# Kernel tuning notes

Hardware: AMD Instinct MI355X
Metric: run time of the kernel (lower is better)

## Reference

```python
import jax, jax.numpy as jnp
import numpy as np

B, C, H, W = 32, 256, 56, 56
NH, WS, SS = 8, 7, 3
N = WS * WS
EPS = 1e-5


def _rel_pos_index(ws):
    ch, cw = np.meshgrid(np.arange(ws), np.arange(ws), indexing='ij')
    coords = np.stack([ch.reshape(-1), cw.reshape(-1)])  # (2, N)
    rel = coords[:, :, None] - coords[:, None, :]        # (2, N, N)
    rel = rel.transpose(1, 2, 0)
    rel[:, :, 0] += ws - 1
    rel[:, :, 1] += ws - 1
    rel[:, :, 0] *= 2 * ws - 1
    return rel.sum(-1)  # (N, N) int


def _attn_mask(Hh, Ww, ws, ss):
    img = np.zeros((Hh, Ww), dtype=np.float32)
    cnt = 0
    for hs in (slice(0, -ws), slice(-ws, -ss), slice(-ss, None)):
        for wsl in (slice(0, -ws), slice(-ws, -ss), slice(-ss, None)):
            img[hs, wsl] = cnt
            cnt += 1
    mw = img.reshape(Hh // ws, ws, Ww // ws, ws).transpose(0, 2, 1, 3).reshape(-1, ws * ws)
    am = mw[:, None, :] - mw[:, :, None]
    return np.where(am != 0, np.float32(-100.0), np.float32(0.0))  # (nW, N, N)

RPI = _rel_pos_index(WS)
AMASK = _attn_mask(H, W, WS, SS)


def _ln(x, w, b):
    mu = x.mean(-1, keepdims=True)
    var = ((x - mu) ** 2).mean(-1, keepdims=True)
    return (x - mu) * jax.lax.rsqrt(var + EPS) * w + b


def setup_inputs() -> dict:
    key = jax.random.key(0)
    ks = jax.random.split(key, 10)
    s = 0.02
    return {
        'x': jax.random.normal(ks[0], (B, C, H, W), jnp.float32),
        'qkv_w': jax.random.normal(ks[1], (3 * C, C), jnp.float32) * s,
        'q_bias': jnp.zeros((C,), jnp.float32),
        'v_bias': jnp.zeros((C,), jnp.float32),
        'proj_w': jax.random.normal(ks[2], (C, C), jnp.float32) * s,
        'proj_b': jnp.zeros((C,), jnp.float32),
        'rpb_table': jax.random.normal(ks[3], ((2 * WS - 1) * (2 * WS - 1), NH), jnp.float32) * s,
        'norm1_w': jnp.ones((C,), jnp.float32),
        'norm1_b': jnp.zeros((C,), jnp.float32),
        'norm2_w': jnp.ones((C,), jnp.float32),
        'norm2_b': jnp.zeros((C,), jnp.float32),
        'fc1_w': jax.random.normal(ks[4], (4 * C, C), jnp.float32) * s,
        'fc1_b': jnp.zeros((4 * C,), jnp.float32),
        'fc2_w': jax.random.normal(ks[5], (C, 4 * C), jnp.float32) * s,
        'fc2_b': jnp.zeros((C,), jnp.float32),
    }


def reference(x, qkv_w, q_bias, v_bias, proj_w, proj_b, rpb_table,
              norm1_w, norm1_b, norm2_w, norm2_b, fc1_w, fc1_b, fc2_w, fc2_b):
    b = x.shape[0]
    hd = C // NH
    scale = hd ** -0.5
    nWh, nWw = H // WS, W // WS
    nW = nWh * nWw

    # (B,C,H,W) -> (B, L, C)
    xs = x.transpose(0, 2, 3, 1).reshape(b, H * W, C)
    shortcut = xs
    xn = _ln(xs, norm1_w, norm1_b).reshape(b, H, W, C)
    # cyclic shift
    xn = jnp.roll(xn, (-SS, -SS), axis=(1, 2))
    # window partition -> (B*nW, N, C)
    xw = xn.reshape(b, nWh, WS, nWw, WS, C).transpose(0, 1, 3, 2, 4, 5).reshape(b * nW, N, C)

    qkv_bias = jnp.concatenate([q_bias, jnp.zeros_like(v_bias), v_bias])
    qkv = xw @ qkv_w.T + qkv_bias                      # (B_, N, 3C)
    qkv = qkv.reshape(b * nW, N, 3, NH, hd).transpose(2, 0, 3, 1, 4)
    q, k, v = qkv[0], qkv[1], qkv[2]                   # (B_, NH, N, hd)

    attn = jnp.einsum('whnd,whmd->whnm', q * scale, k)  # (B_, NH, N, N)
    bias = rpb_table[RPI.reshape(-1)].reshape(N, N, NH).transpose(2, 0, 1)
    attn = attn + bias[None]
    attn = attn.reshape(b, nW, NH, N, N) + jnp.asarray(AMASK)[None, :, None]
    attn = jax.nn.softmax(attn.reshape(b * nW, NH, N, N), axis=-1)

    out = jnp.einsum('whnm,whmd->whnd', attn, v)        # (B_, NH, N, hd)
    out = out.transpose(0, 2, 1, 3).reshape(b * nW, N, C)
    out = out @ proj_w.T + proj_b

    # window reverse + un-shift
    out = out.reshape(b, nWh, nWw, WS, WS, C).transpose(0, 1, 3, 2, 4, 5).reshape(b, H, W, C)
    out = jnp.roll(out, (SS, SS), axis=(1, 2)).reshape(b, H * W, C)

    xs = shortcut + out
    h = _ln(xs, norm2_w, norm2_b)
    h = jax.nn.relu(h @ fc1_w.T + fc1_b) @ fc2_w.T + fc2_b
    xs = xs + h
    return xs.reshape(b, H, W, C).transpose(0, 3, 1, 2)
```

## Files before the change

kernel.cpp:

```cpp
#include <hip/hip_runtime.h>
#include <math.h>

#define EPS 1e-5f

constexpr int Bc = 32, Cc = 256, Hc = 56, Wc = 56;
constexpr int NHc = 8, HDc = 32, WSc = 7, SSc = 3;
constexpr int NTOK = 49;
constexpr int NWIN = 64;
constexpr int Lc = Hc * Wc;
constexpr int Mrows = Bc * NWIN * NTOK;
constexpr int GIMG = 16;
constexpr int NGRP = Bc / GIMG;
constexpr int ROWS_G = GIMG * Lc;
constexpr int WIN_G = GIMG * NWIN;

typedef short bf16x8 __attribute__((ext_vector_type(8)));
typedef float f32x4 __attribute__((ext_vector_type(4)));
typedef unsigned short u16x8 __attribute__((ext_vector_type(8)));
typedef unsigned short u16x4 __attribute__((ext_vector_type(4)));

__device__ __forceinline__ float bf2f(unsigned short u) {
    return __uint_as_float(((unsigned)u) << 16);
}
__device__ __forceinline__ unsigned short f2bf(float f) {
    unsigned x = __float_as_uint(f);
    return (unsigned short)((x + 0x7fffu + ((x >> 16) & 1u)) >> 16);
}
__device__ __forceinline__ void gload_lds16(const void* g, void* l) {
    __builtin_amdgcn_global_load_lds(
        (const __attribute__((address_space(1))) unsigned int*)g,
        (__attribute__((address_space(3))) unsigned int*)l, 16, 0, 0);
}
__device__ __forceinline__ void inv_swz(int bp, int& row, int& ch) {
    int b2 = ((bp >> 2) ^ (bp >> 4)) & 1;
    int b1_ = ((bp >> 1) ^ (bp >> 3)) & 1;
    int b0 = (bp ^ (bp >> 2) ^ (bp >> 4)) & 1;
    int B = (bp & ~7) | (b2 << 2) | (b1_ << 1) | b0;
    row = B >> 2; ch = B & 3;
}

__global__ __launch_bounds__(256) void k_prep(const float* __restrict__ qkv_w,
                                              const float* __restrict__ proj_w,
                                              const float* __restrict__ w1,
                                              const float* __restrict__ w2,
                                              const float* __restrict__ qb,
                                              const float* __restrict__ vb,
                                              unsigned short* __restrict__ qkv_wb,
                                              unsigned short* __restrict__ proj_wb,
                                              unsigned short* __restrict__ w1t,
                                              unsigned short* __restrict__ w2t,
                                              float* __restrict__ qkvb) {
    int i = blockIdx.x * 256 + threadIdx.x;
    if (i < 768) qkvb[i] = (i < 256) ? qb[i] : ((i < 512) ? 0.f : vb[i - 512]);
    if (i < 196608) qkv_wb[i] = f2bf(qkv_w[i]);
    if (i < 65536)  proj_wb[i] = f2bf(proj_w[i]);
    if (i < 262144) {
        int n1 = i >> 8, k1 = i & 255;
        w1t[((n1 >> 4) * 32 + (k1 >> 3)) * 128 + (n1 & 15) * 8 + (k1 & 7)] = f2bf(w1[i]);
        int n2 = i >> 10, k2 = i & 1023;
        w2t[((k2 >> 6) * 32 + (n2 >> 4) * 2 + ((k2 >> 5) & 1)) * 512 +
            ((k2 >> 3) & 3) * 128 + (n2 & 15) * 8 + (k2 & 7)] = f2bf(w2[i]);
    }
}

__global__ __launch_bounds__(256) void k_ln1_part(const float* __restrict__ x,
                                                  const float* __restrict__ n1w,
                                                  const float* __restrict__ n1b,
                                                  unsigned short* __restrict__ xw,
                                                  unsigned short* __restrict__ xres,
                                                  int b0) {
    __shared__ float s[Cc * 57];
    __shared__ float mu[Wc], rs[Wc];
    int bg = blockIdx.x / Hc, h = blockIdx.x % Hc;
    int b = b0 + bg;
    int t = threadIdx.x;
    const float* xp = x + ((size_t)b * Cc) * Lc + h * Wc;
    for (int idx = t; idx < Cc * Wc; idx += 256) {
        int c = idx / Wc, w = idx % Wc;
        s[c * 57 + w] = xp[(size_t)c * Lc + w];
    }
    __syncthreads();
    int lane = t & 63, wv = t >> 6;
    for (int p = wv; p < Wc; p += 4) {
        float sum = 0.f, sq = 0.f;
        #pragma unroll
        for (int k = 0; k < 4; ++k) {
            float v = s[(lane + 64 * k) * 57 + p];
            sum += v; sq += v * v;
        }
        #pragma unroll
        for (int off = 32; off; off >>= 1) {
            sum += __shfl_xor(sum, off);
            sq  += __shfl_xor(sq, off);
        }
        if (lane == 0) {
            float m = sum / Cc;
            mu[p] = m;
            rs[p] = rsqrtf(sq / Cc - m * m + EPS);
        }
    }
    __syncthreads();
    float wc_ = n1w[t], bc_ = n1b[t];
    int hr = (h + Hc - SSc) % Hc;
    int whh = hr / WSc, th = hr % WSc;
    for (int p = 0; p < Wc; ++p) {
        float raw = s[t * 57 + p];
        xres[((size_t)bg * Lc + h * Wc + p) * Cc + t] = f2bf(raw);
        int wr = (p + Wc - SSc) % Wc;
        int www = wr / WSc, tw = wr % WSc;
        int row = (b * NWIN + whh * 8 + www) * NTOK + th * WSc + tw;
        float v = (raw - mu[p]) * rs[p] * wc_ + bc_;
        xw[(size_t)row * Cc + t] = f2bf(v);
    }
}

__global__ __launch_bounds__(256) void k_gemm_mfma(const unsigned short* __restrict__ A,
                                                   const unsigned short* __restrict__ W,
                                                   const float* __restrict__ bias,
                                                   unsigned short* __restrict__ outb,
                                                   int K, int Nd) {
    __shared__ unsigned short As[128 * 32];
    __shared__ unsigned short Bs[128 * 32];
    int t = threadIdx.x;
    int l = t & 63, w = t >> 6;
    int wm = w & 1, wn = w >> 1;
    int m0 = blockIdx.x * 128, n0 = blockIdx.y * 128;
    int lr = l & 15, lg = l >> 4;

    int row0, ch0, row1, ch1;
    inv_swz(w * 128 + l, row0, ch0);
    inv_swz(w * 128 + 64 + l, row1, ch1);
    const unsigned short* gA0 = A + (size_t)(m0 + row0) * K + ch0 * 8;
    const unsigned short* gA1 = A + (size_t)(m0 + row1) * K + ch1 * 8;
    const unsigned short* gB0 = W + (size_t)(n0 + row0) * K + ch0 * 8;
    const unsigned short* gB1 = W + (size_t)(n0 + row1) * K + ch1 * 8;
    unsigned short* lA0 = &As[(w * 128) * 8];
    unsigned short* lA1 = &As[(w * 128 + 64) * 8];
    unsigned short* lB0 = &Bs[(w * 128) * 8];
    unsigned short* lB1 = &Bs[(w * 128 + 64) * 8];

    f32x4 acc[4][4];
    #pragma unroll
    for (int i = 0; i < 4; ++i)
        #pragma unroll
        for (int j = 0; j < 4; ++j)
            acc[i][j] = (f32x4){0.f, 0.f, 0.f, 0.f};

    for (int kt = 0; kt < K; kt += 32) {
        gload_lds16(gA0 + kt, lA0);
        gload_lds16(gA1 + kt, lA1);
        gload_lds16(gB0 + kt, lB0);
        gload_lds16(gB1 + kt, lB1);
        __syncthreads();
        bf16x8 af[4], bfr[4];
        #pragma unroll
        for (int i = 0; i < 4; ++i) {
            int ra = wm * 64 + i * 16 + lr;
            af[i] = *(bf16x8*)&As[(ra * 32 + lg * 8) ^ ((ra & 7) << 3)];
            int rb = wn * 64 + i * 16 + lr;
            bfr[i] = *(bf16x8*)&Bs[(rb * 32 + lg * 8) ^ ((rb & 7) << 3)];
        }
        #pragma unroll
        for (int i = 0; i < 4; ++i)
            #pragma unroll
            for (int j = 0; j < 4; ++j)
                acc[i][j] = __builtin_amdgcn_mfma_f32_16x16x32_bf16(af[i], bfr[j], acc[i][j], 0, 0, 0);
        __syncthreads();
    }

    float bj[4];
    #pragma unroll
    for (int j = 0; j < 4; ++j) bj[j] = bias[n0 + wn * 64 + j * 16 + lr];
    #pragma unroll
    for (int i = 0; i < 4; ++i)
        #pragma unroll
        for (int j = 0; j < 4; ++j) {
            int col = n0 + wn * 64 + j * 16 + lr;
            #pragma unroll
            for (int r = 0; r < 4; ++r) {
                int row = m0 + wm * 64 + i * 16 + lg * 4 + r;
                outb[(size_t)row * Nd + col] = f2bf(acc[i][j][r] + bj[j]);
            }
        }
}

__global__ __launch_bounds__(256) void k_gemm_proj(const unsigned short* __restrict__ A,
                                                   const unsigned short* __restrict__ W,
                                                   const float* __restrict__ bias,
                                                   const unsigned short* __restrict__ xres,
                                                   unsigned short* __restrict__ xs) {
    __shared__ unsigned short As[128 * 32];
    __shared__ unsigned short Bs[128 * 32];
    constexpr int K = 256;
    constexpr int LDA = 768;
    int t = threadIdx.x;
    int l = t & 63, w = t >> 6;
    int wm = w & 1, wn = w >> 1;
    int m0 = blockIdx.x * 128, n0 = blockIdx.y * 128;
    int lr = l & 15, lg = l >> 4;

    int row0, ch0, row1, ch1;
    inv_swz(w * 128 + l, row0, ch0);
    inv_swz(w * 128 + 64 + l, row1, ch1);
    const unsigned short* gA0 = A + (size_t)(m0 + row0) * LDA + ch0 * 8;
    const unsigned short* gA1 = A + (size_t)(m0 + row1) * LDA + ch1 * 8;
    const unsigned short* gB0 = W + (size_t)(n0 + row0) * K + ch0 * 8;
    const unsigned short* gB1 = W + (size_t)(n0 + row1) * K + ch1 * 8;
    unsigned short* lA0 = &As[(w * 128) * 8];
    unsigned short* lA1 = &As[(w * 128 + 64) * 8];
    unsigned short* lB0 = &Bs[(w * 128) * 8];
    unsigned short* lB1 = &Bs[(w * 128 + 64) * 8];

    f32x4 acc[4][4];
    #pragma unroll
    for (int i = 0; i < 4; ++i)
        #pragma unroll
        for (int j = 0; j < 4; ++j)
            acc[i][j] = (f32x4){0.f, 0.f, 0.f, 0.f};

    for (int kt = 0; kt < K; kt += 32) {
        gload_lds16(gA0 + kt, lA0);
        gload_lds16(gA1 + kt, lA1);
        gload_lds16(gB0 + kt, lB0);
        gload_lds16(gB1 + kt, lB1);
        __syncthreads();
        bf16x8 af[4], bfr[4];
        #pragma unroll
        for (int i = 0; i < 4; ++i) {
            int ra = wm * 64 + i * 16 + lr;
            af[i] = *(bf16x8*)&As[(ra * 32 + lg * 8) ^ ((ra & 7) << 3)];
            int rb = wn * 64 + i * 16 + lr;
            bfr[i] = *(bf16x8*)&Bs[(rb * 32 + lg * 8) ^ ((rb & 7) << 3)];
        }
        #pragma unroll
        for (int i = 0; i < 4; ++i)
            #pragma unroll
            for (int j = 0; j < 4; ++j)
                acc[i][j] = __builtin_amdgcn_mfma_f32_16x16x32_bf16(af[i], bfr[j], acc[i][j], 0, 0, 0);
        __syncthreads();
    }

    float bj[4];
    #pragma unroll
    for (int j = 0; j < 4; ++j) bj[j] = bias[n0 + wn * 64 + j * 16 + lr];
    #pragma unroll
    for (int i = 0; i < 4; ++i)
        #pragma unroll
        for (int j = 0; j < 4; ++j) {
            int col = n0 + wn * 64 + j * 16 + lr;
            #pragma unroll
            for (int r = 0; r < 4; ++r) {
                int row = m0 + wm * 64 + i * 16 + lg * 4 + r;
                int wl = row / NTOK, tok = row - wl * NTOK;
                int bg = wl >> 6, wi = wl & 63;
                int hr = (wi >> 3) * 7 + tok / 7;
                int wr = (wi & 7) * 7 + tok % 7;
                int hh = hr + SSc; if (hh >= Hc) hh -= Hc;
                int ww = wr + SSc; if (ww >= Wc) ww -= Wc;
                size_t didx = ((size_t)bg * Lc + hh * Wc + ww) * Cc + col;
                float res = bf2f(xres[didx]);
                xs[didx] = f2bf(res + acc[i][j][r] + bj[j]);
            }
        }
}

__global__ __launch_bounds__(256) void k_attn(unsigned short* __restrict__ qkv,
                                              const float* __restrict__ rpb) {
    __shared__ unsigned short lds[4 * 6144 + 1352];
    unsigned short* rpbs = &lds[4 * 6144];
    int t = threadIdx.x;
    int w = t >> 6, l = t & 63;
    int lr = l & 15, lg = l >> 4;
    unsigned short* wl = &lds[w * 6144];
    unsigned short* Qs = wl;
    unsigned short* Ks = wl + 2048;
    unsigned short* Pm = wl;
    unsigned short* Vt = wl + 4096;

    for (int i = t; i < 1352; i += 256) rpbs[i] = f2bf(rpb[i]);

    int gid = blockIdx.x * 4 + w;
    int b_ = gid >> 3, hh = gid & 7;
    unsigned short* base = qkv + (size_t)b_ * NTOK * 768 + hh * HDc;

    {
        int j = l;
        u16x8 vq[4], vk[4], vv[4];
        if (j < NTOK) {
            const unsigned short* rp = base + j * 768;
            #pragma unroll
            for (int s = 0; s < 4; ++s) {
                vq[s] = *(const u16x8*)(rp + s * 8);
                vk[s] = *(const u16x8*)(rp + 256 + s * 8);
                vv[s] = *(const u16x8*)(rp + 512 + s * 8);
            }
        } else {
            u16x8 z = {0, 0, 0, 0, 0, 0, 0, 0};
            #pragma unroll
            for (int s = 0; s < 4; ++s) { vq[s] = z; vk[s] = z; vv[s] = z; }
        }
        #pragma unroll
        for (int s = 0; s < 4; ++s) {
            int off = (j * 32 + s * 8) ^ ((j & 7) << 3);
            *(u16x8*)&Qs[off] = vq[s];
            *(u16x8*)&Ks[off] = vk[s];
        }
        #pragma unroll
        for (int s = 0; s < 4; ++s)
            #pragma unroll
            for (int e = 0; e < 8; ++e) {
                int d = s * 8 + e;
                Vt[d * 64 + (j ^ ((d & 7) << 3))] = ((unsigned short*)&vv[s])[e];
            }
    }
    __syncthreads();

    bf16x8 aq[4], bk[4];
    #pragma unroll
    for (int mt = 0; mt < 4; ++mt) {
        int row = mt * 16 + lr;
        int off = (row * 32 + lg * 8) ^ ((row & 7) << 3);
        aq[mt] = *(bf16x8*)&Qs[off];
        bk[mt] = *(bf16x8*)&Ks[off];
    }
    f32x4 sc[4][4];
    #pragma unroll
    for (int mt = 0; mt < 4; ++mt)
        #pragma unroll
        for (int nt = 0; nt < 4; ++nt)
            sc[mt][nt] = __builtin_amdgcn_mfma_f32_16x16x32_bf16(
                aq[mt], bk[nt], (f32x4){0.f, 0.f, 0.f, 0.f}, 0, 0, 0);

    const float scale = 0.17677669529663687f;
    int wi = b_ & 63, wh = wi >> 3, wwc = wi & 7;
    int jh[4], jw[4], ridJ[4];
    #pragma unroll
    for (int nt = 0; nt < 4; ++nt) {
        int j = nt * 16 + lr;
        jh[nt] = j / 7; jw[nt] = j - jh[nt] * 7;
        int gh = wh * 7 + jh[nt], gw = wwc * 7 + jw[nt];
        int rh = gh < 49 ? 0 : (gh < 53 ? 1 : 2);
        int rw = gw < 49 ? 0 : (gw < 53 ? 1 : 2);
        ridJ[nt] = rh * 3 + rw;
    }

    float rowrcp[4][4];
    #pragma unroll
    for (int mt = 0; mt < 4; ++mt) {
        #pragma unroll
        for (int r = 0; r < 4; ++r) {
            int i = mt * 16 + lg * 4 + r;
            int ih = i / 7, iw = i - ih * 7;
            int gh = wh * 7 + ih, gw = wwc * 7 + iw;
            int rhI = gh < 49 ? 0 : (gh < 53 ? 1 : 2);
            int rwI = gw < 49 ? 0 : (gw < 53 ? 1 : 2);
            int ridI = rhI * 3 + rwI;
            bool ivalid = (i < NTOK);
            float vals[4];
            float vmax = -1e30f;
            #pragma unroll
            for (int nt = 0; nt < 4; ++nt) {
                int j = nt * 16 + lr;
                float v = -1e30f;
                if (ivalid && j < NTOK) {
                    int rpi = (ih - jh[nt] + 6) * 13 + (iw - jw[nt] + 6);
                    float bv = bf2f(rpbs[rpi * 8 + hh]);
                    float msk = (ridI == ridJ[nt]) ? 0.f : -100.f;
                    v = sc[mt][nt][r] * scale + bv + msk;
                }
                vals[nt] = v;
                vmax = fmaxf(vmax, v);
            }
            #pragma unroll
            for (int off = 1; off < 16; off <<= 1)
                vmax = fmaxf(vmax, __shfl_xor(vmax, off));
            float s = 0.f;
            unsigned short pb[4];
            #pragma unroll
            for (int nt = 0; nt < 4; ++nt) {
                float e = (vals[nt] > -1e29f) ? __expf(vals[nt] - vmax) : 0.f;
                s += e;
                pb[nt] = f2bf(e);
            }
            #pragma unroll
            for (int off = 1; off < 16; off <<= 1)
                s += __shfl_xor(s, off);
            rowrcp[mt][r] = 1.f / s;
            #pragma unroll
            for (int nt = 0; nt < 4; ++nt) {
                int j = nt * 16 + lr;
                Pm[(i * 64 + j) ^ ((i & 7) << 3)] = pb[nt];
            }
        }
    }

    f32x4 o[4][2];
    #pragma unroll
    for (int mt = 0; mt < 4; ++mt)
        #pragma unroll
        for (int nt = 0; nt < 2; ++nt)
            o[mt][nt] = (f32x4){0.f, 0.f, 0.f, 0.f};
    #pragma unroll
    for (int ks = 0; ks < 2; ++ks) {
        bf16x8 ap[4], bv2[2];
        #pragma unroll
        for (int mt = 0; mt < 4; ++mt) {
            int row = mt * 16 + lr;
            ap[mt] = *(bf16x8*)&Pm[(row * 64 + ks * 32 + lg * 8) ^ ((row & 7) << 3)];
        }
        #pragma unroll
        for (int nt = 0; nt < 2; ++nt) {
            int n = nt * 16 + lr;
            bv2[nt] = *(bf16x8*)&Vt[(n * 64 + ks * 32 + lg * 8) ^ ((n & 7) << 3)];
        }
        #pragma unroll
        for (int mt = 0; mt < 4; ++mt)
            #pragma unroll
            for (int nt = 0; nt < 2; ++nt)
                o[mt][nt] = __builtin_amdgcn_mfma_f32_16x16x32_bf16(ap[mt], bv2[nt], o[mt][nt], 0, 0, 0);
    }

    #pragma unroll
    for (int mt = 0; mt < 4; ++mt)
        #pragma unroll
        for (int r = 0; r < 4; ++r) {
            int i = mt * 16 + lg * 4 + r;
            if (i < NTOK) {
                float rc = rowrcp[mt][r];
                #pragma unroll
                for (int nt = 0; nt < 2; ++nt) {
                    int d = nt * 16 + lr;
                    qkv[((size_t)b_ * NTOK + i) * 768 + hh * HDc + d] = f2bf(o[mt][nt][r] * rc);
                }
            }
        }
}

#define HIDX(m, c) (((m) * 64 + (c)) ^ (((m) & 7) << 3))
__global__ __launch_bounds__(512) void k_mlp_fused(const unsigned short* __restrict__ xs,
                                                   const float* __restrict__ n2w,
                                                   const float* __restrict__ n2b,
                                                   const unsigned short* __restrict__ w1t,
                                                   const float* __restrict__ b1,
                                                   const unsigned short* __restrict__ w2t,
                                                   const float* __restrict__ b2,
                                                   float* __restrict__ out) {
    __shared__ unsigned short w1s[16384];
    __shared__ unsigned short hid[8192];
    int t = threadIdx.x;
    int l = t & 63, w = t >> 6;
    int wm = w >> 1, wn = w & 1;
    int lr = l & 15, lg = l >> 4;
    int m0 = blockIdx.x * 128;

    bf16x8 xf[2][8];
    {
        #pragma unroll
        for (int mf = 0; mf < 2; ++mf) {
            int row = m0 + wm * 32 + mf * 16 + lr;
            const unsigned short* xrow = xs + (size_t)row * Cc;
            u16x8 raw[8];
            float sum = 0.f, sq = 0.f;
            #pragma unroll
            for (int ks = 0; ks < 8; ++ks) {
                raw[ks] = *(const u16x8*)(xrow + ks * 32 + lg * 8);
                #pragma unroll
                for (int e = 0; e < 8; ++e) {
                    float f = bf2f(raw[ks][e]);
                    sum += f; sq += f * f;
                }
            }
            sum += __shfl_xor(sum, 16); sq += __shfl_xor(sq, 16);
            sum += __shfl_xor(sum, 32); sq += __shfl_xor(sq, 32);
            float mu = sum / Cc;
            float rsg = rsqrtf(sq / Cc - mu * mu + EPS);
            #pragma unroll
            for (int ks = 0; ks < 8; ++ks) {
                #pragma unroll
                for (int e = 0; e < 8; ++e) {
                    int c = ks * 32 + lg * 8 + e;
                    float nv = (bf2f(raw[ks][e]) - mu) * rsg * n2w[c] + n2b[c];
                    ((unsigned short*)&xf[mf][ks])[e] = f2bf(nv);
                }
            }
        }
    }

    f32x4 acc2[2][8];
    #pragma unroll
    for (int mf = 0; mf < 2; ++mf)
        #pragma unroll
        for (int nf = 0; nf < 8; ++nf)
            acc2[mf][nf] = (f32x4){0.f, 0.f, 0.f, 0.f};

    u16x8 p1[4];
    #pragma unroll
    for (int i = 0; i < 4; ++i)
        p1[i] = *(const u16x8*)(w1t + (i * 512 + t) * 8);

    for (int ch = 0; ch < 16; ++ch) {
        #pragma unroll
        for (int i = 0; i < 4; ++i)
            *(u16x8*)&w1s[(i * 512 + t) * 8] = p1[i];
        __syncthreads();
        if (ch < 15) {
            const unsigned short* n1 = w1t + (ch + 1) * 16384;
            #pragma unroll
            for (int i = 0; i < 4; ++i)
                p1[i] = *(const u16x8*)(n1 + (i * 512 + t) * 8);
        }
        {
            f32x4 acc1[2][2];
            #pragma unroll
            for (int ht = 0; ht < 2; ++ht)
                #pragma unroll
                for (int mf = 0; mf < 2; ++mf)
                    acc1[ht][mf] = (f32x4){0.f, 0.f, 0.f, 0.f};
            #pragma unroll
            for (int ks = 0; ks < 8; ++ks) {
                bf16x8 wfr[2];
                #pragma unroll
                for (int ht = 0; ht < 2; ++ht)
                    wfr[ht] = *(const bf16x8*)&w1s[(wn * 2 + ht) * 4096 + ks * 512 + l * 8];
                #pragma unroll
                for (int ht = 0; ht < 2; ++ht) {
                    acc1[ht][0] = __builtin_amdgcn_mfma_f32_16x16x32_bf16(wfr[ht], xf[0][ks], acc1[ht][0], 0, 0, 0);
                    acc1[ht][1] = __builtin_amdgcn_mfma_f32_16x16x32_bf16(wfr[ht], xf[1][ks], acc1[ht][1], 0, 0, 0);
                }
            }
            #pragma unroll
            for (int ht = 0; ht < 2; ++ht) {
                float b1v[4];
                #pragma unroll
                for (int r = 0; r < 4; ++r)
                    b1v[r] = b1[ch * 64 + (wn * 2 + ht) * 16 + lg * 4 + r];
                #pragma unroll
                for (int mf = 0; mf < 2; ++mf) {
                    u16x4 pk;
                    #pragma unroll
                    for (int r = 0; r < 4; ++r)
                        pk[r] = f2bf(fmaxf(acc1[ht][mf][r] + b1v[r], 0.f));
                    int m = wm * 32 + mf * 16 + lr;
                    int off = m * 64 + ((((wn * 2 + ht) * 16) + lg * 4) ^ ((m & 7) << 3));
                    *(u16x4*)&hid[off] = pk;
                }
            }
        }
        __syncthreads();
        {
            bf16x8 a[2][2];
            #pragma unroll
            for (int mf = 0; mf < 2; ++mf)
                #pragma unroll
                for (int ks = 0; ks < 2; ++ks) {
                    int m = wm * 32 + mf * 16 + lr;
                    a[mf][ks] = *(const bf16x8*)&hid[HIDX(m, ks * 32 + lg * 8)];
                }
            const unsigned short* w2c = w2t + ch * 16384;
            #pragma unroll
            for (int ks = 0; ks < 2; ++ks)
                #pragma unroll
                for (int nf = 0; nf < 8; ++nf) {
                    int nt = wn * 8 + nf;
                    bf16x8 bfr = *(const bf16x8*)&w2c[(nt * 2 + ks) * 512 + l * 8];
                    acc2[0][nf] = __builtin_amdgcn_mfma_f32_16x16x32_bf16(a[0][ks], bfr, acc2[0][nf], 0, 0, 0);
                    acc2[1][nf] = __builtin_amdgcn_mfma_f32_16x16x32_bf16(a[1][ks], bfr, acc2[1][nf], 0, 0, 0);
                }
        }
        __syncthreads();
    }

    int b0i = m0 / Lc, l0 = m0 % Lc;
    #pragma unroll
    for (int nf = 0; nf < 8; ++nf) {
        int c = wn * 128 + nf * 16 + lr;
        float b2c = b2[c];
        #pragma unroll
        for (int mf = 0; mf < 2; ++mf)
            #pragma unroll
            for (int r = 0; r < 4; ++r) {
                int m = wm * 32 + mf * 16 + lg * 4 + r;
                float res = bf2f(xs[(size_t)(m0 + m) * Cc + c]);
                int lm = l0 + m;
                int bi = b0i + (lm >= Lc);
                if (lm >= Lc) lm -= Lc;
                out[((size_t)bi * Cc + c) * Lc + lm] = acc2[mf][nf][r] + b2c + res;
            }
    }
}

extern "C" void kernel_launch(void* const* d_in, const int* in_sizes, int n_in,
                              void* d_out, int out_size, void* d_ws, size_t ws_size,
                              hipStream_t stream) {
    const float* x      = (const float*)d_in[0];
    const float* qkv_w  = (const float*)d_in[1];
    const float* q_bias = (const float*)d_in[2];
    const float* v_bias = (const float*)d_in[3];
    const float* proj_w = (const float*)d_in[4];
    const float* proj_b = (const float*)d_in[5];
    const float* rpb    = (const float*)d_in[6];
    const float* n1w    = (const float*)d_in[7];
    const float* n1b    = (const float*)d_in[8];
    const float* n2w    = (const float*)d_in[9];
    const float* n2b    = (const float*)d_in[10];
    const float* w1     = (const float*)d_in[11];
    const float* b1     = (const float*)d_in[12];
    const float* w2     = (const float*)d_in[13];
    const float* b2     = (const float*)d_in[14];

    char* ws = (char*)d_ws;
    const size_t SZ_BF16 = (size_t)Mrows * Cc * 2;
    unsigned short* xw      = (unsigned short*)ws;
    float*          qkvb    = (float*)(ws + SZ_BF16);
    unsigned short* qkv_wb  = (unsigned short*)(ws + SZ_BF16 + 3072);
    unsigned short* proj_wb = qkv_wb + 196608;
    unsigned short* w1t     = proj_wb + 65536;
    unsigned short* w2t     = w1t + 262144;

    unsigned short* qkv_s  = (unsigned short*)d_out;
    unsigned short* xres_s = qkv_s + (size_t)ROWS_G * 768;

    k_prep<<<1024, 256, 0, stream>>>(qkv_w, proj_w, w1, w2, q_bias, v_bias,
                                     qkv_wb, proj_wb, w1t, w2t, qkvb);

    for (int g = 0; g < NGRP; ++g) {
        unsigned short* xw_g = xw + (size_t)g * ROWS_G * Cc;
        k_ln1_part<<<GIMG * Hc, 256, 0, stream>>>(x, n1w, n1b, xw, xres_s, g * GIMG);
        k_gemm_mfma<<<dim3(ROWS_G / 128, 768 / 128), 256, 0, stream>>>(
            xw_g, qkv_wb, qkvb, qkv_s, 256, 768);
        k_attn<<<WIN_G * NHc / 4, 256, 0, stream>>>(qkv_s, rpb);
        k_gemm_proj<<<dim3(ROWS_G / 128, 2), 256, 0, stream>>>(
            qkv_s, proj_wb, proj_b, xres_s, xw_g);
    }

    k_mlp_fused<<<Mrows / 128, 512, 0, stream>>>(xw, n2w, n2b, w1t, b1, w2t, b2,
                                                 (float*)d_out);
}
```

Measured before the change: 616.6 us.

## Restructure fused MLP to per-wave rows with register-shuffled hidden and LDS-staged W2

The fused MLP kernel now gives each wave 16 full rows and keeps the ReLU hidden activations in registers, moving them into MFMA A-operand layout with lane shuffles instead of an LDS round trip. FC2 weight chunks are staged in LDS and prefetched through registers, and FC1 weights are loaded straight into LDS with global_load_lds. This removes the hidden-buffer LDS write/read and one barrier per chunk, at the cost of more accumulators per wave and more shuffles. Separately, the two GEMM kernels remap blockIdx.x with an XCD-aware swizzle so that neighbouring tiles share an XCD's L2.

```diff
diff --git a/kernel.cpp b/kernel.cpp
--- a/kernel.cpp
+++ b/kernel.cpp
@@ -37,6 +37,10 @@
     int b0 = (bp ^ (bp >> 2) ^ (bp >> 4)) & 1;
     int B = (bp & ~7) | (b2 << 2) | (b1_ << 1) | b0;
     row = B >> 2; ch = B & 3;
+}
+__device__ __forceinline__ int xcd_swz(int bx, int nwg) {
+    int cpx = nwg >> 3;
+    return (bx & 7) * cpx + (bx >> 3);
 }
 
 __global__ __launch_bounds__(256) void k_prep(const float* __restrict__ qkv_w,
@@ -124,7 +128,8 @@
     int t = threadIdx.x;
     int l = t & 63, w = t >> 6;
     int wm = w & 1, wn = w >> 1;
-    int m0 = blockIdx.x * 128, n0 = blockIdx.y * 128;
+    int bx = xcd_swz(blockIdx.x, gridDim.x);
+    int m0 = bx * 128, n0 = blockIdx.y * 128;
     int lr = l & 15, lg = l >> 4;
 
     int row0, ch0, row1, ch1;
@@ -196,7 +201,8 @@
     int t = threadIdx.x;
     int l = t & 63, w = t >> 6;
     int wm = w & 1, wn = w >> 1;
-    int m0 = blockIdx.x * 128, n0 = blockIdx.y * 128;
+    int bx = xcd_swz(blockIdx.x, gridDim.x);
+    int m0 = bx * 128, n0 = blockIdx.y * 128;
     int lr = l & 15, lg = l >> 4;
 
     int row0, ch0, row1, ch1;
@@ -436,7 +442,6 @@
         }
 }
 
-#define HIDX(m, c) (((m) * 64 + (c)) ^ (((m) & 7) << 3))
 __global__ __launch_bounds__(512) void k_mlp_fused(const unsigned short* __restrict__ xs,
                                                    const float* __restrict__ n2w,
                                                    const float* __restrict__ n2b,
@@ -446,146 +451,138 @@
                                                    const float* __restrict__ b2,
                                                    float* __restrict__ out) {
     __shared__ unsigned short w1s[16384];
-    __shared__ unsigned short hid[8192];
+    __shared__ unsigned short w2s[16384];
     int t = threadIdx.x;
     int l = t & 63, w = t >> 6;
-    int wm = w >> 1, wn = w & 1;
     int lr = l & 15, lg = l >> 4;
     int m0 = blockIdx.x * 128;
-
-    bf16x8 xf[2][8];
+    int mrow = m0 + w * 16 + lr;
+
+    bf16x8 xf[8];
     {
-        #pragma unroll
-        for (int mf = 0; mf < 2; ++mf) {
-            int row = m0 + wm * 32 + mf * 16 + lr;
-            const unsigned short* xrow = xs + (size_t)row * Cc;
-            u16x8 raw[8];
-            float sum = 0.f, sq = 0.f;
-            #pragma unroll
-            for (int ks = 0; ks < 8; ++ks) {
-                raw[ks] = *(const u16x8*)(xrow + ks * 32 + lg * 8);
-                #pragma unroll
-                for (int e = 0; e < 8; ++e) {
-                    float f = bf2f(raw[ks][e]);
-                    sum += f; sq += f * f;
-                }
-            }
-            sum += __shfl_xor(sum, 16); sq += __shfl_xor(sq, 16);
-            sum += __shfl_xor(sum, 32); sq += __shfl_xor(sq, 32);
-            float mu = sum / Cc;
-            float rsg = rsqrtf(sq / Cc - mu * mu + EPS);
-            #pragma unroll
-            for (int ks = 0; ks < 8; ++ks) {
-                #pragma unroll
-                for (int e = 0; e < 8; ++e) {
-                    int c = ks * 32 + lg * 8 + e;
-                    float nv = (bf2f(raw[ks][e]) - mu) * rsg * n2w[c] + n2b[c];
-                    ((unsigned short*)&xf[mf][ks])[e] = f2bf(nv);
-                }
-            }
-        }
-    }
-
-    f32x4 acc2[2][8];
-    #pragma unroll
-    for (int mf = 0; mf < 2; ++mf)
-        #pragma unroll
-        for (int nf = 0; nf < 8; ++nf)
-            acc2[mf][nf] = (f32x4){0.f, 0.f, 0.f, 0.f};
-
-    u16x8 p1[4];
+        const unsigned short* xrow = xs + (size_t)mrow * Cc;
+        u16x8 raw[8];
+        float sum = 0.f, sq = 0.f;
+        #pragma unroll
+        for (int ks = 0; ks < 8; ++ks) {
+            raw[ks] = *(const u16x8*)(xrow + ks * 32 + lg * 8);
+            #pragma unroll
+            for (int e = 0; e < 8; ++e) {
+                float f = bf2f(raw[ks][e]);
+                sum += f; sq += f * f;
+            }
+        }
+        sum += __shfl_xor(sum, 16); sq += __shfl_xor(sq, 16);
+        sum += __shfl_xor(sum, 32); sq += __shfl_xor(sq, 32);
+        float mu = sum / Cc;
+        float rsg = rsqrtf(sq / Cc - mu * mu + EPS);
+        #pragma unroll
+        for (int ks = 0; ks < 8; ++ks) {
+            #pragma unroll
+            for (int e = 0; e < 8; ++e) {
+                int c = ks * 32 + lg * 8 + e;
+                float nv = (bf2f(raw[ks][e]) - mu) * rsg * n2w[c] + n2b[c];
+                ((unsigned short*)&xf[ks])[e] = f2bf(nv);
+            }
+        }
+    }
+
     #pragma unroll
     for (int i = 0; i < 4; ++i)
-        p1[i] = *(const u16x8*)(w1t + (i * 512 + t) * 8);
+        gload_lds16(w1t + (size_t)(i * 512 + t) * 8, &w1s[(i * 512 + (w << 6)) * 8]);
+    u16x8 p2[4];
+    #pragma unroll
+    for (int i = 0; i < 4; ++i)
+        p2[i] = *(const u16x8*)(w2t + (size_t)(i * 512 + t) * 8);
+    __syncthreads();
+
+    f32x4 acc2[16];
+    #pragma unroll
+    for (int nf = 0; nf < 16; ++nf)
+        acc2[nf] = (f32x4){0.f, 0.f, 0.f, 0.f};
 
     for (int ch = 0; ch < 16; ++ch) {
+        f32x4 acc1[4];
+        #pragma unroll
+        for (int ht = 0; ht < 4; ++ht)
+            acc1[ht] = (f32x4){0.f, 0.f, 0.f, 0.f};
+        #pragma unroll
+        for (int ks = 0; ks < 8; ++ks) {
+            #pragma unroll
+            for (int ht = 0; ht < 4; ++ht) {
+                bf16x8 wfr = *(const bf16x8*)&w1s[ht * 4096 + ks * 512 + l * 8];
+                acc1[ht] = __builtin_amdgcn_mfma_f32_16x16x32_bf16(wfr, xf[ks], acc1[ht], 0, 0, 0);
+            }
+        }
+        unsigned px[4][2];
+        #pragma unroll
+        for (int ht = 0; ht < 4; ++ht) {
+            unsigned short pk[4];
+            #pragma unroll
+            for (int r = 0; r < 4; ++r)
+                pk[r] = f2bf(fmaxf(acc1[ht][r] + b1[ch * 64 + ht * 16 + lg * 4 + r], 0.f));
+            px[ht][0] = (unsigned)pk[0] | ((unsigned)pk[1] << 16);
+            px[ht][1] = (unsigned)pk[2] | ((unsigned)pk[3] << 16);
+        }
         #pragma unroll
         for (int i = 0; i < 4; ++i)
-            *(u16x8*)&w1s[(i * 512 + t) * 8] = p1[i];
+            *(u16x8*)&w2s[(i * 512 + t) * 8] = p2[i];
+        if (ch < 15) {
+            const unsigned short* n2p = w2t + (size_t)(ch + 1) * 16384;
+            #pragma unroll
+            for (int i = 0; i < 4; ++i)
+                p2[i] = *(const u16x8*)(n2p + (size_t)(i * 512 + t) * 8);
+        }
         __syncthreads();
         if (ch < 15) {
-            const unsigned short* n1 = w1t + (ch + 1) * 16384;
+            const unsigned short* n1p = w1t + (size_t)(ch + 1) * 16384;
             #pragma unroll
             for (int i = 0; i < 4; ++i)
-                p1[i] = *(const u16x8*)(n1 + (i * 512 + t) * 8);
-        }
-        {
-            f32x4 acc1[2][2];
-            #pragma unroll
-            for (int ht = 0; ht < 2; ++ht)
-                #pragma unroll
-                for (int mf = 0; mf < 2; ++mf)
-                    acc1[ht][mf] = (f32x4){0.f, 0.f, 0.f, 0.f};
-            #pragma unroll
-            for (int ks = 0; ks < 8; ++ks) {
-                bf16x8 wfr[2];
-                #pragma unroll
-                for (int ht = 0; ht < 2; ++ht)
-                    wfr[ht] = *(const bf16x8*)&w1s[(wn * 2 + ht) * 4096 + ks * 512 + l * 8];
-                #pragma unroll
-                for (int ht = 0; ht < 2; ++ht) {
-                    acc1[ht][0] = __builtin_amdgcn_mfma_f32_16x16x32_bf16(wfr[ht], xf[0][ks], acc1[ht][0], 0, 0, 0);
-                    acc1[ht][1] = __builtin_amdgcn_mfma_f32_16x16x32_bf16(wfr[ht], xf[1][ks], acc1[ht][1], 0, 0, 0);
-                }
-            }
-            #pragma unroll
-            for (int ht = 0; ht < 2; ++ht) {
-                float b1v[4];
-                #pragma unroll
-                for (int r = 0; r < 4; ++r)
-                    b1v[r] = b1[ch * 64 + (wn * 2 + ht) * 16 + lg * 4 + r];
-                #pragma unroll
-                for (int mf = 0; mf < 2; ++mf) {
-                    u16x4 pk;
-                    #pragma unroll
-                    for (int r = 0; r < 4; ++r)
-                        pk[r] = f2bf(fmaxf(acc1[ht][mf][r] + b1v[r], 0.f));
-                    int m = wm * 32 + mf * 16 + lr;
-                    int off = m * 64 + ((((wn * 2 + ht) * 16) + lg * 4) ^ ((m & 7) << 3));
-                    *(u16x4*)&hid[off] = pk;
-                }
+                gload_lds16(n1p + (size_t)(i * 512 + t) * 8, &w1s[(i * 512 + (w << 6)) * 8]);
+        }
+        #pragma unroll
+        for (int ks2 = 0; ks2 < 2; ++ks2) {
+            int s0 = lr + ((lg & 1) << 5);
+            int s1 = s0 + 16;
+            int hA = ks2 * 2, hB = hA + 1;
+            unsigned a0 = (unsigned)__shfl((int)px[hA][0], s0);
+            unsigned a1 = (unsigned)__shfl((int)px[hA][1], s0);
+            unsigned a2 = (unsigned)__shfl((int)px[hA][0], s1);
+            unsigned a3 = (unsigned)__shfl((int)px[hA][1], s1);
+            unsigned c0 = (unsigned)__shfl((int)px[hB][0], s0);
+            unsigned c1 = (unsigned)__shfl((int)px[hB][1], s0);
+            unsigned c2 = (unsigned)__shfl((int)px[hB][0], s1);
+            unsigned c3 = (unsigned)__shfl((int)px[hB][1], s1);
+            bool hiT = (lg >> 1) != 0;
+            union { unsigned u[4]; bf16x8 v; } cvt;
+            cvt.u[0] = hiT ? c0 : a0;
+            cvt.u[1] = hiT ? c1 : a1;
+            cvt.u[2] = hiT ? c2 : a2;
+            cvt.u[3] = hiT ? c3 : a3;
+            bf16x8 af = cvt.v;
+            #pragma unroll
+            for (int nf = 0; nf < 16; ++nf) {
+                bf16x8 bfr = *(const bf16x8*)&w2s[(nf * 2 + ks2) * 512 + l * 8];
+                acc2[nf] = __builtin_amdgcn_mfma_f32_16x16x32_bf16(af, bfr, acc2[nf], 0, 0, 0);
             }
         }
         __syncthreads();
-        {
-            bf16x8 a[2][2];
-            #pragma unroll
-            for (int mf = 0; mf < 2; ++mf)
-                #pragma unroll
-                for (int ks = 0; ks < 2; ++ks) {
-                    int m = wm * 32 + mf * 16 + lr;
-                    a[mf][ks] = *(const bf16x8*)&hid[HIDX(m, ks * 32 + lg * 8)];
-                }
-            const unsigned short* w2c = w2t + ch * 16384;
-            #pragma unroll
-            for (int ks = 0; ks < 2; ++ks)
-                #pragma unroll
-                for (int nf = 0; nf < 8; ++nf) {
-                    int nt = wn * 8 + nf;
-                    bf16x8 bfr = *(const bf16x8*)&w2c[(nt * 2 + ks) * 512 + l * 8];
-                    acc2[0][nf] = __builtin_amdgcn_mfma_f32_16x16x32_bf16(a[0][ks], bfr, acc2[0][nf], 0, 0, 0);
-                    acc2[1][nf] = __builtin_amdgcn_mfma_f32_16x16x32_bf16(a[1][ks], bfr, acc2[1][nf], 0, 0, 0);
-                }
-        }
-        __syncthreads();
     }
 
     int b0i = m0 / Lc, l0 = m0 % Lc;
     #pragma unroll
-    for (int nf = 0; nf < 8; ++nf) {
-        int c = wn * 128 + nf * 16 + lr;
+    for (int nf = 0; nf < 16; ++nf) {
+        int c = nf * 16 + lr;
         float b2c = b2[c];
         #pragma unroll
-        for (int mf = 0; mf < 2; ++mf)
-            #pragma unroll
-            for (int r = 0; r < 4; ++r) {
-                int m = wm * 32 + mf * 16 + lg * 4 + r;
-                float res = bf2f(xs[(size_t)(m0 + m) * Cc + c]);
-                int lm = l0 + m;
-                int bi = b0i + (lm >= Lc);
-                if (lm >= Lc) lm -= Lc;
-                out[((size_t)bi * Cc + c) * Lc + lm] = acc2[mf][nf][r] + b2c + res;
-            }
+        for (int r = 0; r < 4; ++r) {
+            int m = w * 16 + lg * 4 + r;
+            float res = bf2f(xs[(size_t)(m0 + m) * Cc + c]);
+            int lm = l0 + m;
+            int bi = b0i + (lm >= Lc);
+            if (lm >= Lc) lm -= Lc;
+            out[((size_t)bi * Cc + c) * Lc + lm] = acc2[nf][r] + b2c + res;
+        }
     }
 }
 
```

Measured after the change: 589.5 us. 1.05x faster.
